# Optimization experiments

Measured on AMD Instinct MI355X. Metric: run time of the kernel, lower is better.

## Reference

```python
import jax, jax.numpy as jnp
import numpy as np


def quaternion_to_matrix(q):
    # q: [..., 4] in (w, x, y, z) convention (pytorch3d quaternion_to_matrix)
    r, i, j, k = q[..., 0], q[..., 1], q[..., 2], q[..., 3]
    two_s = 2.0 / jnp.sum(q * q, axis=-1)
    m = jnp.stack([
        1 - two_s * (j * j + k * k), two_s * (i * j - k * r), two_s * (i * k + j * r),
        two_s * (i * j + k * r), 1 - two_s * (i * i + k * k), two_s * (j * k - i * r),
        two_s * (i * k - j * r), two_s * (j * k + i * r), 1 - two_s * (i * i + j * j),
    ], axis=-1)
    return m.reshape(q.shape[:-1] + (3, 3))


def setup_inputs() -> dict:
    key = jax.random.key(0)
    k1, k2, k3, k4 = jax.random.split(key, 4)
    B, K, P = 512, 8192, 4096
    softEncodePred = jax.random.normal(k1, (B, K), dtype=jnp.float32)
    oriHistogramMap = jax.random.normal(k2, (B, K, 4), dtype=jnp.float32)
    oriHistogramMap = oriHistogramMap / jnp.linalg.norm(oriHistogramMap, axis=-1, keepdims=True)
    gt = jax.random.normal(k3, (B, 4), dtype=jnp.float32)
    gt = gt / jnp.linalg.norm(gt, axis=-1, keepdims=True)
    point = jax.random.normal(k4, (B, P, 3), dtype=jnp.float32)
    return {"softEncodePred": softEncodePred, "oriHistogramMap": oriHistogramMap,
            "gt": gt, "point": point}


def reference(softEncodePred, oriHistogramMap, gt, point):
    # softmax over histogram bins -> per-bin weights [B, K]
    w = jax.nn.softmax(softEncodePred, axis=-1)
    # Davenport q-method: A = sum_k w_k q_k q_k^T  (4x4 symmetric per sample)
    A = jnp.einsum('bk,bki,bkj->bij', w, oriHistogramMap, oriHistogramMap)
    _, v = jnp.linalg.eigh(A)           # ascending eigenvalues
    q_pred = v[:, :, -1]                # eigenvector of largest eigenvalue [B, 4]
    q_pred = q_pred / jnp.linalg.norm(q_pred, axis=-1, keepdims=True)
    # rotation matrices [B, 3, 3]; sign ambiguity of q is irrelevant (R quadratic in q)
    rm_gt = quaternion_to_matrix(gt)
    rm_pred = quaternion_to_matrix(q_pred)
    # original: row-vector times matrix, p @ R, per point
    point_gt = jnp.einsum('bpi,bij->bpj', point, rm_gt)
    point_pred = jnp.einsum('bpi,bij->bpj', point, rm_pred)
    diff = point_pred - point_gt                       # [B, P, 3]
    return jnp.mean(jnp.linalg.norm(diff, axis=-1))    # mean over all B*P points
```

## Files before the change

### kernel.cpp

```cpp
#include <hip/hip_runtime.h>
#include <math.h>

#define KDIM 8192
#define BATCH 512
#define PDIM 4096

__global__ __launch_bounds__(256) void k_softmax_accum(
    const float* __restrict__ sep, const float* __restrict__ ohm,
    float* __restrict__ Abuf)
{
    __shared__ float srow[KDIM];
    __shared__ float red[64];
    const int b    = blockIdx.x;
    const int tid  = threadIdx.x;
    const int lane = tid & 63, wave = tid >> 6;

    const float4* row4  = (const float4*)(sep + (size_t)b * KDIM);
    float4*       srow4 = (float4*)srow;
    float mx = -INFINITY;
    for (int i = tid; i < KDIM / 4; i += 256) {
        float4 v = row4[i];
        srow4[i] = v;
        mx = fmaxf(mx, fmaxf(fmaxf(v.x, v.y), fmaxf(v.z, v.w)));
    }
    #pragma unroll
    for (int off = 32; off > 0; off >>= 1)
        mx = fmaxf(mx, __shfl_down(mx, off, 64));
    if (lane == 0) red[wave] = mx;
    __syncthreads();
    if (tid == 0) red[0] = fmaxf(fmaxf(red[0], red[1]), fmaxf(red[2], red[3]));
    __syncthreads();
    mx = red[0];

    float acc[11];
    #pragma unroll
    for (int i = 0; i < 11; i++) acc[i] = 0.f;

    const float4* q4 = (const float4*)(ohm + (size_t)b * KDIM * 4);
    for (int k = tid; k < KDIM; k += 256) {
        float4 q = q4[k];
        float e  = __expf(srow[k] - mx);
        float ex = e * q.x, ey = e * q.y, ez = e * q.z, ew = e * q.w;
        acc[0]  += e;
        acc[1]  += ex * q.x; acc[2] += ex * q.y; acc[3] += ex * q.z; acc[4] += ex * q.w;
        acc[5]  += ey * q.y; acc[6] += ey * q.z; acc[7] += ey * q.w;
        acc[8]  += ez * q.z; acc[9] += ez * q.w;
        acc[10] += ew * q.w;
    }

    __syncthreads();
    #pragma unroll
    for (int i = 0; i < 11; i++) {
        float s = acc[i];
        #pragma unroll
        for (int off = 32; off > 0; off >>= 1)
            s += __shfl_down(s, off, 64);
        if (lane == 0) red[wave * 11 + i] = s;
    }
    __syncthreads();
    if (tid < 11)
        Abuf[b * 12 + tid] = red[tid] + red[11 + tid] + red[22 + tid] + red[33 + tid];
}

__global__ void k_eig(const float* __restrict__ Abuf, const float* __restrict__ gt,
                      float* __restrict__ Rbuf)
{
    int b = blockIdx.x * blockDim.x + threadIdx.x;
    if (b >= BATCH) return;
    const float* a = Abuf + b * 12;
    double inv = 1.0 / (double)a[0];
    double A[4][4];
    A[0][0] = a[1] * inv; A[0][1] = a[2] * inv; A[0][2] = a[3] * inv; A[0][3] = a[4] * inv;
    A[1][1] = a[5] * inv; A[1][2] = a[6] * inv; A[1][3] = a[7] * inv;
    A[2][2] = a[8] * inv; A[2][3] = a[9] * inv; A[3][3] = a[10] * inv;
    A[1][0] = A[0][1]; A[2][0] = A[0][2]; A[3][0] = A[0][3];
    A[2][1] = A[1][2]; A[3][1] = A[1][3]; A[3][2] = A[2][3];

    double V[4][4];
    for (int i = 0; i < 4; i++)
        for (int j = 0; j < 4; j++) V[i][j] = (i == j) ? 1.0 : 0.0;

    for (int sweep = 0; sweep < 15; ++sweep) {
        double off = A[0][1]*A[0][1] + A[0][2]*A[0][2] + A[0][3]*A[0][3]
                   + A[1][2]*A[1][2] + A[1][3]*A[1][3] + A[2][3]*A[2][3];
        if (off < 1e-26) break;
        for (int p = 0; p < 3; p++) for (int q = p + 1; q < 4; q++) {
            double apq = A[p][q];
            if (fabs(apq) < 1e-30) continue;
            double theta = (A[q][q] - A[p][p]) / (2.0 * apq);
            double t = copysign(1.0, theta) / (fabs(theta) + sqrt(theta * theta + 1.0));
            double c = 1.0 / sqrt(t * t + 1.0);
            double s = t * c;
            for (int i = 0; i < 4; i++) {
                double aip = A[i][p], aiq = A[i][q];
                A[i][p] = c * aip - s * aiq;
                A[i][q] = s * aip + c * aiq;
            }
            for (int i = 0; i < 4; i++) {
                double api = A[p][i], aqi = A[q][i];
                A[p][i] = c * api - s * aqi;
                A[q][i] = s * api + c * aqi;
            }
            for (int i = 0; i < 4; i++) {
                double vip = V[i][p], viq = V[i][q];
                V[i][p] = c * vip - s * viq;
                V[i][q] = s * vip + c * viq;
            }
        }
    }
    int best = 0;
    for (int j = 1; j < 4; j++) if (A[j][j] > A[best][best]) best = j;
    double qr = V[0][best], qi = V[1][best], qj = V[2][best], qk = V[3][best];
    double two_s = 2.0 / (qr*qr + qi*qi + qj*qj + qk*qk);

    float* R = Rbuf + b * 18;
    R[0] = (float)(1.0 - two_s * (qj*qj + qk*qk));
    R[1] = (float)(two_s * (qi*qj - qk*qr));
    R[2] = (float)(two_s * (qi*qk + qj*qr));
    R[3] = (float)(two_s * (qi*qj + qk*qr));
    R[4] = (float)(1.0 - two_s * (qi*qi + qk*qk));
    R[5] = (float)(two_s * (qj*qk - qi*qr));
    R[6] = (float)(two_s * (qi*qk - qj*qr));
    R[7] = (float)(two_s * (qj*qk + qi*qr));
    R[8] = (float)(1.0 - two_s * (qi*qi + qj*qj));
    double gr = gt[b*4+0], gi = gt[b*4+1], gj = gt[b*4+2], gk = gt[b*4+3];
    double gs = 2.0 / (gr*gr + gi*gi + gj*gj + gk*gk);
    R[9]  = (float)(1.0 - gs * (gj*gj + gk*gk));
    R[10] = (float)(gs * (gi*gj - gk*gr));
    R[11] = (float)(gs * (gi*gk + gj*gr));
    R[12] = (float)(gs * (gi*gj + gk*gr));
    R[13] = (float)(1.0 - gs * (gi*gi + gk*gk));
    R[14] = (float)(gs * (gj*gk - gi*gr));
    R[15] = (float)(gs * (gi*gk - gj*gr));
    R[16] = (float)(gs * (gj*gk + gi*gr));
    R[17] = (float)(1.0 - gs * (gi*gi + gj*gj));
}

__global__ __launch_bounds__(256) void k_points(
    const float* __restrict__ point, const float* __restrict__ Rbuf,
    float* __restrict__ partial)
{
    const int blk   = blockIdx.x;
    const int b     = blk >> 2;
    const int chunk = blk & 3;
    const int tid   = threadIdx.x;
    const int lane  = tid & 63, wave = tid >> 6;
    __shared__ float red[4];

    const float* R = Rbuf + b * 18;
    float rp[9], rg[9];
    #pragma unroll
    for (int i = 0; i < 9; i++) { rp[i] = R[i]; rg[i] = R[9 + i]; }

    const float4* base = (const float4*)(point + ((size_t)b * PDIM + chunk * 1024) * 3);
    float4 v0 = base[tid * 3 + 0];
    float4 v1 = base[tid * 3 + 1];
    float4 v2 = base[tid * 3 + 2];
    float px[4] = { v0.x, v0.w, v1.z, v2.y };
    float py[4] = { v0.y, v1.x, v1.w, v2.z };
    float pz[4] = { v0.z, v1.y, v2.x, v2.w };

    float sum = 0.f;
    #pragma unroll
    for (int t = 0; t < 4; t++) {
        float x = px[t], y = py[t], z = pz[t];
        float ax = x*rp[0] + y*rp[3] + z*rp[6];
        float ay = x*rp[1] + y*rp[4] + z*rp[7];
        float az = x*rp[2] + y*rp[5] + z*rp[8];
        float bx = x*rg[0] + y*rg[3] + z*rg[6];
        float by = x*rg[1] + y*rg[4] + z*rg[7];
        float bz = x*rg[2] + y*rg[5] + z*rg[8];
        float dx = ax - bx, dy = ay - by, dz = az - bz;
        sum += sqrtf(dx*dx + dy*dy + dz*dz);
    }
    #pragma unroll
    for (int off = 32; off > 0; off >>= 1)
        sum += __shfl_down(sum, off, 64);
    if (lane == 0) red[wave] = sum;
    __syncthreads();
    if (tid == 0) partial[blk] = red[0] + red[1] + red[2] + red[3];
}

__global__ __launch_bounds__(256) void k_final(
    const float* __restrict__ partial, float* __restrict__ out)
{
    const int tid  = threadIdx.x;
    const int lane = tid & 63, wave = tid >> 6;
    __shared__ double red[4];
    double s = 0.0;
    for (int i = tid; i < 2048; i += 256) s += (double)partial[i];
    #pragma unroll
    for (int off = 32; off > 0; off >>= 1)
        s += __shfl_down(s, off, 64);
    if (lane == 0) red[wave] = s;
    __syncthreads();
    if (tid == 0)
        out[0] = (float)((red[0] + red[1] + red[2] + red[3]) /
                         (double)((size_t)BATCH * PDIM));
}

extern "C" void kernel_launch(void* const* d_in, const int* in_sizes, int n_in,
                              void* d_out, int out_size, void* d_ws, size_t ws_size,
                              hipStream_t stream)
{
    const float* sep   = (const float*)d_in[0];
    const float* ohm   = (const float*)d_in[1];
    const float* gt    = (const float*)d_in[2];
    const float* point = (const float*)d_in[3];
    float* out = (float*)d_out;

    float* Abuf = (float*)d_ws;
    float* Rbuf = Abuf + BATCH * 12;
    float* Pbuf = Rbuf + BATCH * 18;

    k_softmax_accum<<<BATCH, 256, 0, stream>>>(sep, ohm, Abuf);
    k_eig<<<2, 256, 0, stream>>>(Abuf, gt, Rbuf);
    k_points<<<2048, 256, 0, stream>>>(point, Rbuf, Pbuf);
    k_final<<<1, 256, 0, stream>>>(Pbuf, out);
}
```

Baseline: 167.6 us.

## Split softmax accumulation across four chunks per sample with online-max merge

The softmax-weighted accumulation now runs as four blocks per sample, each covering a 2048-bin chunk. Each block emits its local max and partial sums, and the eigen kernel merges them with exp rescaling, which raises the number of blocks available to saturate memory bandwidth. The eigen kernel also runs at a smaller block size across more blocks, caps Jacobi sweeps at 10, and precomputes the difference of the two rotation matrices so the points kernel does one 3x3 transform per point. The cost is an extra rescaling step in the merge and a lower cap on Jacobi iterations.

New measurement: 150.2 us. 1.12x faster.

```diff
diff --git a/kernel.cpp b/kernel.cpp
--- a/kernel.cpp
+++ b/kernel.cpp
@@ -4,23 +4,27 @@
 #define KDIM 8192
 #define BATCH 512
 #define PDIM 4096
-
-__global__ __launch_bounds__(256) void k_softmax_accum(
+#define CHUNK 2048
+
+__global__ __launch_bounds__(256) void k_partial(
     const float* __restrict__ sep, const float* __restrict__ ohm,
-    float* __restrict__ Abuf)
-{
-    __shared__ float srow[KDIM];
+    float* __restrict__ Cbuf)
+{
+    __shared__ float ss[CHUNK];
     __shared__ float red[64];
-    const int b    = blockIdx.x;
+    const int blk  = blockIdx.x;
+    const int b    = blk >> 2;
+    const int c    = blk & 3;
     const int tid  = threadIdx.x;
     const int lane = tid & 63, wave = tid >> 6;
 
-    const float4* row4  = (const float4*)(sep + (size_t)b * KDIM);
-    float4*       srow4 = (float4*)srow;
+    const float4* s4  = (const float4*)(sep + (size_t)b * KDIM + c * CHUNK);
+    float4*       ss4 = (float4*)ss;
     float mx = -INFINITY;
-    for (int i = tid; i < KDIM / 4; i += 256) {
-        float4 v = row4[i];
-        srow4[i] = v;
+    #pragma unroll
+    for (int i = 0; i < CHUNK / 4 / 256; i++) {
+        float4 v = s4[tid + i * 256];
+        ss4[tid + i * 256] = v;
         mx = fmaxf(mx, fmaxf(fmaxf(v.x, v.y), fmaxf(v.z, v.w)));
     }
     #pragma unroll
@@ -28,18 +32,18 @@
         mx = fmaxf(mx, __shfl_down(mx, off, 64));
     if (lane == 0) red[wave] = mx;
     __syncthreads();
-    if (tid == 0) red[0] = fmaxf(fmaxf(red[0], red[1]), fmaxf(red[2], red[3]));
-    __syncthreads();
-    mx = red[0];
+    mx = fmaxf(fmaxf(red[0], red[1]), fmaxf(red[2], red[3]));
 
     float acc[11];
     #pragma unroll
     for (int i = 0; i < 11; i++) acc[i] = 0.f;
 
-    const float4* q4 = (const float4*)(ohm + (size_t)b * KDIM * 4);
-    for (int k = tid; k < KDIM; k += 256) {
+    const float4* q4 = (const float4*)(ohm + ((size_t)b * KDIM + c * CHUNK) * 4);
+    #pragma unroll
+    for (int j = 0; j < CHUNK / 256; j++) {
+        const int k = j * 256 + tid;
         float4 q = q4[k];
-        float e  = __expf(srow[k] - mx);
+        float e  = __expf(ss[k] - mx);
         float ex = e * q.x, ey = e * q.y, ez = e * q.z, ew = e * q.w;
         acc[0]  += e;
         acc[1]  += ex * q.x; acc[2] += ex * q.y; acc[3] += ex * q.z; acc[4] += ex * q.w;
@@ -55,24 +59,42 @@
         #pragma unroll
         for (int off = 32; off > 0; off >>= 1)
             s += __shfl_down(s, off, 64);
-        if (lane == 0) red[wave * 11 + i] = s;
+        if (lane == 0) red[wave * 12 + i] = s;
     }
     __syncthreads();
     if (tid < 11)
-        Abuf[b * 12 + tid] = red[tid] + red[11 + tid] + red[22 + tid] + red[33 + tid];
-}
-
-__global__ void k_eig(const float* __restrict__ Abuf, const float* __restrict__ gt,
-                      float* __restrict__ Rbuf)
-{
-    int b = blockIdx.x * blockDim.x + threadIdx.x;
+        Cbuf[blk * 12 + tid] = red[tid] + red[12 + tid] + red[24 + tid] + red[36 + tid];
+    if (tid == 11)
+        Cbuf[blk * 12 + 11] = mx;
+}
+
+__global__ __launch_bounds__(64) void k_eig(
+    const float* __restrict__ Cbuf, const float* __restrict__ gt,
+    float* __restrict__ Dbuf)
+{
+    int b = blockIdx.x * 64 + threadIdx.x;
     if (b >= BATCH) return;
-    const float* a = Abuf + b * 12;
-    double inv = 1.0 / (double)a[0];
+    const float* C = Cbuf + b * 48;
+
+    float mg = fmaxf(fmaxf(C[11], C[23]), fmaxf(C[35], C[47]));
+    double sum_e = 0.0;
+    double M[10];
+    #pragma unroll
+    for (int i = 0; i < 10; i++) M[i] = 0.0;
+    #pragma unroll
+    for (int c = 0; c < 4; c++) {
+        const float* cc = C + c * 12;
+        double f = exp((double)(cc[11] - mg));
+        sum_e += f * (double)cc[0];
+        #pragma unroll
+        for (int i = 0; i < 10; i++) M[i] += f * (double)cc[1 + i];
+    }
+    double inv = 1.0 / sum_e;
+
     double A[4][4];
-    A[0][0] = a[1] * inv; A[0][1] = a[2] * inv; A[0][2] = a[3] * inv; A[0][3] = a[4] * inv;
-    A[1][1] = a[5] * inv; A[1][2] = a[6] * inv; A[1][3] = a[7] * inv;
-    A[2][2] = a[8] * inv; A[2][3] = a[9] * inv; A[3][3] = a[10] * inv;
+    A[0][0] = M[0]*inv; A[0][1] = M[1]*inv; A[0][2] = M[2]*inv; A[0][3] = M[3]*inv;
+    A[1][1] = M[4]*inv; A[1][2] = M[5]*inv; A[1][3] = M[6]*inv;
+    A[2][2] = M[7]*inv; A[2][3] = M[8]*inv; A[3][3] = M[9]*inv;
     A[1][0] = A[0][1]; A[2][0] = A[0][2]; A[3][0] = A[0][3];
     A[2][1] = A[1][2]; A[3][1] = A[1][3]; A[3][2] = A[2][3];
 
@@ -80,7 +102,7 @@
     for (int i = 0; i < 4; i++)
         for (int j = 0; j < 4; j++) V[i][j] = (i == j) ? 1.0 : 0.0;
 
-    for (int sweep = 0; sweep < 15; ++sweep) {
+    for (int sweep = 0; sweep < 10; ++sweep) {
         double off = A[0][1]*A[0][1] + A[0][2]*A[0][2] + A[0][3]*A[0][3]
                    + A[1][2]*A[1][2] + A[1][3]*A[1][3] + A[2][3]*A[2][3];
         if (off < 1e-26) break;
@@ -89,55 +111,47 @@
             if (fabs(apq) < 1e-30) continue;
             double theta = (A[q][q] - A[p][p]) / (2.0 * apq);
             double t = copysign(1.0, theta) / (fabs(theta) + sqrt(theta * theta + 1.0));
-            double c = 1.0 / sqrt(t * t + 1.0);
-            double s = t * c;
+            double cth = 1.0 / sqrt(t * t + 1.0);
+            double sth = t * cth;
             for (int i = 0; i < 4; i++) {
                 double aip = A[i][p], aiq = A[i][q];
-                A[i][p] = c * aip - s * aiq;
-                A[i][q] = s * aip + c * aiq;
+                A[i][p] = cth * aip - sth * aiq;
+                A[i][q] = sth * aip + cth * aiq;
             }
             for (int i = 0; i < 4; i++) {
                 double api = A[p][i], aqi = A[q][i];
-                A[p][i] = c * api - s * aqi;
-                A[q][i] = s * api + c * aqi;
+                A[p][i] = cth * api - sth * aqi;
+                A[q][i] = sth * api + cth * aqi;
             }
             for (int i = 0; i < 4; i++) {
                 double vip = V[i][p], viq = V[i][q];
-                V[i][p] = c * vip - s * viq;
-                V[i][q] = s * vip + c * viq;
+                V[i][p] = cth * vip - sth * viq;
+                V[i][q] = sth * vip + cth * viq;
             }
         }
     }
     int best = 0;
     for (int j = 1; j < 4; j++) if (A[j][j] > A[best][best]) best = j;
     double qr = V[0][best], qi = V[1][best], qj = V[2][best], qk = V[3][best];
-    double two_s = 2.0 / (qr*qr + qi*qi + qj*qj + qk*qk);
-
-    float* R = Rbuf + b * 18;
-    R[0] = (float)(1.0 - two_s * (qj*qj + qk*qk));
-    R[1] = (float)(two_s * (qi*qj - qk*qr));
-    R[2] = (float)(two_s * (qi*qk + qj*qr));
-    R[3] = (float)(two_s * (qi*qj + qk*qr));
-    R[4] = (float)(1.0 - two_s * (qi*qi + qk*qk));
-    R[5] = (float)(two_s * (qj*qk - qi*qr));
-    R[6] = (float)(two_s * (qi*qk - qj*qr));
-    R[7] = (float)(two_s * (qj*qk + qi*qr));
-    R[8] = (float)(1.0 - two_s * (qi*qi + qj*qj));
+    double ps = 2.0 / (qr*qr + qi*qi + qj*qj + qk*qk);
+
     double gr = gt[b*4+0], gi = gt[b*4+1], gj = gt[b*4+2], gk = gt[b*4+3];
     double gs = 2.0 / (gr*gr + gi*gi + gj*gj + gk*gk);
-    R[9]  = (float)(1.0 - gs * (gj*gj + gk*gk));
-    R[10] = (float)(gs * (gi*gj - gk*gr));
-    R[11] = (float)(gs * (gi*gk + gj*gr));
-    R[12] = (float)(gs * (gi*gj + gk*gr));
-    R[13] = (float)(1.0 - gs * (gi*gi + gk*gk));
-    R[14] = (float)(gs * (gj*gk - gi*gr));
-    R[15] = (float)(gs * (gi*gk - gj*gr));
-    R[16] = (float)(gs * (gj*gk + gi*gr));
-    R[17] = (float)(1.0 - gs * (gi*gi + gj*gj));
+
+    float* D = Dbuf + b * 9;
+    D[0] = (float)((1.0 - ps*(qj*qj + qk*qk)) - (1.0 - gs*(gj*gj + gk*gk)));
+    D[1] = (float)((ps*(qi*qj - qk*qr))       - (gs*(gi*gj - gk*gr)));
+    D[2] = (float)((ps*(qi*qk + qj*qr))       - (gs*(gi*gk + gj*gr)));
+    D[3] = (float)((ps*(qi*qj + qk*qr))       - (gs*(gi*gj + gk*gr)));
+    D[4] = (float)((1.0 - ps*(qi*qi + qk*qk)) - (1.0 - gs*(gi*gi + gk*gk)));
+    D[5] = (float)((ps*(qj*qk - qi*qr))       - (gs*(gj*gk - gi*gr)));
+    D[6] = (float)((ps*(qi*qk - qj*qr))       - (gs*(gi*gk - gj*gr)));
+    D[7] = (float)((ps*(qj*qk + qi*qr))       - (gs*(gj*gk + gi*gr)));
+    D[8] = (float)((1.0 - ps*(qi*qi + qj*qj)) - (1.0 - gs*(gi*gi + gj*gj)));
 }
 
 __global__ __launch_bounds__(256) void k_points(
-    const float* __restrict__ point, const float* __restrict__ Rbuf,
+    const float* __restrict__ point, const float* __restrict__ Dbuf,
     float* __restrict__ partial)
 {
     const int blk   = blockIdx.x;
@@ -147,10 +161,10 @@
     const int lane  = tid & 63, wave = tid >> 6;
     __shared__ float red[4];
 
-    const float* R = Rbuf + b * 18;
-    float rp[9], rg[9];
-    #pragma unroll
-    for (int i = 0; i < 9; i++) { rp[i] = R[i]; rg[i] = R[9 + i]; }
+    const float* Dp = Dbuf + b * 9;
+    float d[9];
+    #pragma unroll
+    for (int i = 0; i < 9; i++) d[i] = Dp[i];
 
     const float4* base = (const float4*)(point + ((size_t)b * PDIM + chunk * 1024) * 3);
     float4 v0 = base[tid * 3 + 0];
@@ -164,13 +178,9 @@
     #pragma unroll
     for (int t = 0; t < 4; t++) {
         float x = px[t], y = py[t], z = pz[t];
-        float ax = x*rp[0] + y*rp[3] + z*rp[6];
-        float ay = x*rp[1] + y*rp[4] + z*rp[7];
-        float az = x*rp[2] + y*rp[5] + z*rp[8];
-        float bx = x*rg[0] + y*rg[3] + z*rg[6];
-        float by = x*rg[1] + y*rg[4] + z*rg[7];
-        float bz = x*rg[2] + y*rg[5] + z*rg[8];
-        float dx = ax - bx, dy = ay - by, dz = az - bz;
+        float dx = x*d[0] + y*d[3] + z*d[6];
+        float dy = x*d[1] + y*d[4] + z*d[7];
+        float dz = x*d[2] + y*d[5] + z*d[8];
         sum += sqrtf(dx*dx + dy*dy + dz*dz);
     }
     #pragma unroll
@@ -209,12 +219,12 @@
     const float* point = (const float*)d_in[3];
     float* out = (float*)d_out;
 
-    float* Abuf = (float*)d_ws;
-    float* Rbuf = Abuf + BATCH * 12;
-    float* Pbuf = Rbuf + BATCH * 18;
-
-    k_softmax_accum<<<BATCH, 256, 0, stream>>>(sep, ohm, Abuf);
-    k_eig<<<2, 256, 0, stream>>>(Abuf, gt, Rbuf);
-    k_points<<<2048, 256, 0, stream>>>(point, Rbuf, Pbuf);
+    float* Cbuf = (float*)d_ws;
+    float* Dbuf = Cbuf + BATCH * 4 * 12;
+    float* Pbuf = Dbuf + BATCH * 9;
+
+    k_partial<<<BATCH * 4, 256, 0, stream>>>(sep, ohm, Cbuf);
+    k_eig<<<8, 64, 0, stream>>>(Cbuf, gt, Dbuf);
+    k_points<<<2048, 256, 0, stream>>>(point, Dbuf, Pbuf);
     k_final<<<1, 256, 0, stream>>>(Pbuf, out);
 }
```
